# Performance work log

Hardware: AMD Instinct MI355X
Metric: run time of the kernel (lower is better)

## Reference

```python
import jax, jax.numpy as jnp
import numpy as np

KH, KW = 3, 3
STRIDE, PAD, DIL = 1, 1, 1
GROUPS, DG = 1, 1
B, C, H, W = 4, 64, 96, 96
O = 64
K = KH * KW


def setup_inputs() -> dict:
    key = jax.random.key(0)
    k1, k2, k3, k4 = jax.random.split(key, 4)
    x = jax.random.normal(k1, (B, C, H, W), dtype=jnp.float32)
    offset = jax.random.normal(k2, (B, DG * 2 * K, H, W), dtype=jnp.float32)
    mask = jax.random.uniform(k3, (B, DG * K, H, W), dtype=jnp.float32)
    stdv = 1.0 / np.sqrt(C * KH * KW)
    weight = jax.random.uniform(k4, (O, C // GROUPS, KH, KW), dtype=jnp.float32,
                                minval=-stdv, maxval=stdv)
    bias = jnp.zeros((O,), dtype=jnp.float32)
    return {"x": x, "offset": offset, "mask": mask, "weight": weight, "bias": bias}


def _dcn(x, offset, mask, weight, bias):
    Bc, Cc, Hc, Wc = x.shape
    Ho = (Hc + 2 * PAD - DIL * (KH - 1) - 1) // STRIDE + 1
    Wo = (Wc + 2 * PAD - DIL * (KW - 1) - 1) // STRIDE + 1
    Cg = Cc // DG
    dt = x.dtype

    # offset channels per deform group: [k, (y,x)] interleaved (mmcv layout)
    off = offset.reshape(Bc, DG, K, 2, Ho, Wo)
    off_y, off_x = off[:, :, :, 0], off[:, :, :, 1]          # [B,DG,K,Ho,Wo]
    m = mask.reshape(Bc, DG, K, Ho, Wo)

    ky = (jnp.arange(K) // KW).astype(dt) * DIL               # kernel tap dy
    kx = (jnp.arange(K) % KW).astype(dt) * DIL                # kernel tap dx
    base_y = (jnp.arange(Ho) * STRIDE - PAD).astype(dt)
    base_x = (jnp.arange(Wo) * STRIDE - PAD).astype(dt)
    py = base_y[None, None, None, :, None] + ky[None, None, :, None, None] + off_y
    px = base_x[None, None, None, None, :] + kx[None, None, :, None, None] + off_x

    y0 = jnp.floor(py)
    x0 = jnp.floor(px)
    ly = py - y0
    lx = px - x0
    y0i = y0.astype(jnp.int32)
    x0i = x0.astype(jnp.int32)

    x_flat = x.reshape(Bc, DG, Cg, Hc * Wc)

    def gather(yi, xi):
        # zero-padding semantics: out-of-range corners contribute 0
        valid = ((yi >= 0) & (yi < Hc) & (xi >= 0) & (xi < Wc)).astype(dt)
        idx = jnp.clip(yi, 0, Hc - 1) * Wc + jnp.clip(xi, 0, Wc - 1)
        idx_b = jnp.broadcast_to(idx.reshape(Bc, DG, 1, K * Ho * Wo),
                                 (Bc, DG, Cg, K * Ho * Wo))
        vals = jnp.take_along_axis(x_flat, idx_b, axis=3)
        return vals.reshape(Bc, DG, Cg, K, Ho, Wo), valid

    v00, m00 = gather(y0i, x0i)
    v01, m01 = gather(y0i, x0i + 1)
    v10, m10 = gather(y0i + 1, x0i)
    v11, m11 = gather(y0i + 1, x0i + 1)

    w00 = ((1 - ly) * (1 - lx) * m00)[:, :, None]             # [B,DG,1,K,Ho,Wo]
    w01 = ((1 - ly) * lx * m01)[:, :, None]
    w10 = (ly * (1 - lx) * m10)[:, :, None]
    w11 = (ly * lx * m11)[:, :, None]

    sampled = v00 * w00 + v01 * w01 + v10 * w10 + v11 * w11   # bilinear
    sampled = sampled * m[:, :, None]                         # mask modulation
    s = sampled.reshape(Bc, Cc, K, Ho, Wo)

    out = jnp.einsum('ock,bckhw->bohw', weight.reshape(O, Cc, K), s)
    return out + bias[None, :, None, None]


def reference(x, offset, mask, weight, bias):
    return _dcn(x, offset, mask, weight, bias)
```

## Files before the change

### kernel.cpp

```cpp
#include <hip/hip_runtime.h>

#define Bn 4
#define Cn 64
#define Hn 96
#define Wn 96
#define On 64
#define Kn 9
#define HWn (Hn*Wn)
#define NT 256
#define TW (Wn/16)
#define NTILES (Bn*Hn*TW)
#define NBLK (NTILES/4)

typedef __attribute__((ext_vector_type(8))) short bf16x8;
typedef __attribute__((ext_vector_type(4))) float f32x4;

__device__ __forceinline__ unsigned short f2bf(float f) {
    unsigned u = __float_as_uint(f);
    u += 0x7FFFu + ((u >> 16) & 1u);
    return (unsigned short)(u >> 16);
}
__device__ __forceinline__ float bf2f(unsigned short h) {
    return __uint_as_float((unsigned)h << 16);
}

__global__ void wtrans2_kernel(const float* __restrict__ w, unsigned short* __restrict__ wbfA) {
    int i = blockIdx.x * NT + threadIdx.x;
    if (i < 18 * 4 * 64 * 8) {
        int j  = i & 7;
        int l  = (i >> 3) & 63;
        int ot = (i >> 9) & 3;
        int t  = i >> 11;
        int o  = ot * 16 + (l & 15);
        int kp = t * 32 + (l >> 4) * 8 + j;
        wbfA[i] = f2bf(w[(o * Cn + (kp & 63)) * Kn + (kp >> 6)]);
    }
}

__global__ __launch_bounds__(NT) void xtrans_kernel(const float* __restrict__ x,
                                                    unsigned short* __restrict__ xT) {
    __shared__ unsigned short tile[Cn * Wn];
    const int tid = threadIdx.x;
    const int b = blockIdx.x / Hn;
    const int h = blockIdx.x - b * Hn;
    #pragma unroll
    for (int i = 0; i < (Cn * Wn) / NT; ++i) {
        int e = i * NT + tid;
        int c = e / Wn, w = e - c * Wn;
        tile[c * Wn + w] = f2bf(x[(((size_t)b * Cn + c) * Hn + h) * Wn + w]);
    }
    __syncthreads();
    #pragma unroll
    for (int i = 0; i < (Wn * 8) / NT; ++i) {
        int s = i * NT + tid;
        int w = s >> 3, g = s & 7;
        unsigned short hh[8];
        #pragma unroll
        for (int j = 0; j < 8; ++j) hh[j] = tile[(g * 8 + j) * Wn + w];
        uint4 pk;
        pk.x = hh[0] | ((unsigned)hh[1] << 16);
        pk.y = hh[2] | ((unsigned)hh[3] << 16);
        pk.z = hh[4] | ((unsigned)hh[5] << 16);
        pk.w = hh[6] | ((unsigned)hh[7] << 16);
        *(uint4*)&xT[(((size_t)b * Hn + h) * Wn + w) * Cn + g * 8] = pk;
    }
}

__global__ __launch_bounds__(NT) void dcn3_kernel(
    const unsigned short* __restrict__ xT, const float* __restrict__ offset,
    const float* __restrict__ mask, const float* __restrict__ bias,
    const unsigned short* __restrict__ wbfA, float* __restrict__ out)
{
    __shared__ float4 lwv[4 * Kn * 16];
    __shared__ int4   liv[4 * Kn * 16];

    const int tid = threadIdx.x;
    const int p = blockIdx.x;
    const int v = (p & 7) * (NBLK / 8) + (p >> 3);

    for (int e = tid; e < 4 * Kn * 16; e += NT) {
        int w   = e / (Kn * 16);
        int r   = e - w * (Kn * 16);
        int k   = r >> 4;
        int n   = r & 15;
        int T   = v * 4 + w;
        int b   = T / (Hn * TW);
        int rem = T - b * (Hn * TW);
        int ho  = rem / TW;
        int wt  = rem - ho * TW;
        int wo  = wt * 16 + n;

        float oy = offset[((b * (2*Kn) + 2*k    ) * Hn + ho) * Wn + wo];
        float ox = offset[((b * (2*Kn) + 2*k + 1) * Hn + ho) * Wn + wo];
        float mm = mask  [((b * Kn + k) * Hn + ho) * Wn + wo];
        float py = (float)(ho - 1 + (k / 3)) + oy;
        float px = (float)(wo - 1 + (k % 3)) + ox;
        float y0f = floorf(py), x0f = floorf(px);
        float ly = py - y0f, lx = px - x0f;
        int y0 = (int)y0f, x0i = (int)x0f;
        int y1 = y0 + 1,   x1i = x0i + 1;
        float vy0 = (y0  >= 0 && y0  < Hn) ? 1.f : 0.f;
        float vy1 = (y1  >= 0 && y1  < Hn) ? 1.f : 0.f;
        float vx0 = (x0i >= 0 && x0i < Wn) ? 1.f : 0.f;
        float vx1 = (x1i >= 0 && x1i < Wn) ? 1.f : 0.f;
        int cy0 = min(max(y0, 0),  Hn-1), cy1 = min(max(y1, 0),  Hn-1);
        int cx0 = min(max(x0i, 0), Wn-1), cx1 = min(max(x1i, 0), Wn-1);
        float4 wv;
        wv.x = (1.f - ly) * (1.f - lx) * mm * vy0 * vx0;
        wv.y = (1.f - ly) * lx         * mm * vy0 * vx1;
        wv.z = ly         * (1.f - lx) * mm * vy1 * vx0;
        wv.w = ly         * lx         * mm * vy1 * vx1;
        lwv[e] = wv;
        liv[e] = make_int4(cy0 * Wn + cx0, cy0 * Wn + cx1,
                           cy1 * Wn + cx0, cy1 * Wn + cx1);
    }
    __syncthreads();

    const int wave = tid >> 6;
    const int lane = tid & 63;
    const int n    = lane & 15;
    const int quad = lane >> 4;
    const int qo   = quad * 8;

    const int T  = v * 4 + wave;
    const int b  = T / (Hn * TW);
    int rem      = T - b * (Hn * TW);
    const int ho = rem / TW;
    const int wt = rem - ho * TW;
    const int wo0 = wt * 16;

    const unsigned short* xb = xT + (size_t)b * HWn * Cn;
    const bf16x8* Af = (const bf16x8*)wbfA;

    f32x4 acc[4] = {{0.f,0.f,0.f,0.f},{0.f,0.f,0.f,0.f},
                    {0.f,0.f,0.f,0.f},{0.f,0.f,0.f,0.f}};

    #pragma unroll
    for (int k = 0; k < Kn; ++k) {
        const int te = (wave * Kn + k) * 16 + n;
        float4 wv = lwv[te];
        int4   iv = liv[te];

        const unsigned short* r0 = xb + ((size_t)iv.x << 6) + qo;
        const unsigned short* r1 = xb + ((size_t)iv.y << 6) + qo;
        const unsigned short* r2 = xb + ((size_t)iv.z << 6) + qo;
        const unsigned short* r3 = xb + ((size_t)iv.w << 6) + qo;
        bf16x8 v00 = *(const bf16x8*)r0,  v01 = *(const bf16x8*)(r0 + 32);
        bf16x8 v10 = *(const bf16x8*)r1,  v11 = *(const bf16x8*)(r1 + 32);
        bf16x8 v20 = *(const bf16x8*)r2,  v21 = *(const bf16x8*)(r2 + 32);
        bf16x8 v30 = *(const bf16x8*)r3,  v31 = *(const bf16x8*)(r3 + 32);

        bf16x8 b0, b1;
        #pragma unroll
        for (int j = 0; j < 8; ++j) {
            float f0 = wv.x * bf2f((unsigned short)v00[j]) + wv.y * bf2f((unsigned short)v10[j])
                     + wv.z * bf2f((unsigned short)v20[j]) + wv.w * bf2f((unsigned short)v30[j]);
            float f1 = wv.x * bf2f((unsigned short)v01[j]) + wv.y * bf2f((unsigned short)v11[j])
                     + wv.z * bf2f((unsigned short)v21[j]) + wv.w * bf2f((unsigned short)v31[j]);
            b0[j] = (short)f2bf(f0);
            b1[j] = (short)f2bf(f1);
        }

        const int t0 = 2 * k, t1 = 2 * k + 1;
        #pragma unroll
        for (int ot = 0; ot < 4; ++ot) {
            bf16x8 a0 = Af[(t0 * 4 + ot) * 64 + lane];
            acc[ot] = __builtin_amdgcn_mfma_f32_16x16x32_bf16(a0, b0, acc[ot], 0, 0, 0);
        }
        #pragma unroll
        for (int ot = 0; ot < 4; ++ot) {
            bf16x8 a1 = Af[(t1 * 4 + ot) * 64 + lane];
            acc[ot] = __builtin_amdgcn_mfma_f32_16x16x32_bf16(a1, b1, acc[ot], 0, 0, 0);
        }
    }

    #pragma unroll
    for (int ot = 0; ot < 4; ++ot) {
        #pragma unroll
        for (int r = 0; r < 4; ++r) {
            int o = ot * 16 + quad * 4 + r;
            out[(((size_t)b * On + o) * Hn + ho) * Wn + wo0 + n] = acc[ot][r] + bias[o];
        }
    }
}

__global__ __launch_bounds__(NT) void dcn_fallback_kernel(
    const float* __restrict__ x, const float* __restrict__ offset,
    const float* __restrict__ mask, const float* __restrict__ weight,
    const float* __restrict__ bias, float* __restrict__ out)
{
    int idx = blockIdx.x * NT + threadIdx.x;
    if (idx >= Bn * On * HWn) return;
    int wo = idx % Wn;
    int ho = (idx / Wn) % Hn;
    int o  = (idx / HWn) % On;
    int b  = idx / (On * HWn);
    float s = bias[o];
    for (int k = 0; k < Kn; ++k) {
        float oy = offset[((b * (2*Kn) + 2*k    ) * Hn + ho) * Wn + wo];
        float ox = offset[((b * (2*Kn) + 2*k + 1) * Hn + ho) * Wn + wo];
        float mm = mask  [((b * Kn + k) * Hn + ho) * Wn + wo];
        float py = (float)(ho - 1 + (k / 3)) + oy;
        float px = (float)(wo - 1 + (k % 3)) + ox;
        float y0f = floorf(py), x0f = floorf(px);
        float ly = py - y0f, lx = px - x0f;
        int y0 = (int)y0f, x0i = (int)x0f, y1 = y0 + 1, x1i = x0i + 1;
        float vy0 = (y0  >= 0 && y0  < Hn) ? 1.f : 0.f;
        float vy1 = (y1  >= 0 && y1  < Hn) ? 1.f : 0.f;
        float vx0 = (x0i >= 0 && x0i < Wn) ? 1.f : 0.f;
        float vx1 = (x1i >= 0 && x1i < Wn) ? 1.f : 0.f;
        int cy0 = min(max(y0, 0),  Hn-1), cy1 = min(max(y1, 0),  Hn-1);
        int cx0 = min(max(x0i, 0), Wn-1), cx1 = min(max(x1i, 0), Wn-1);
        float w0 = (1.f-ly)*(1.f-lx)*mm*vy0*vx0, w1 = (1.f-ly)*lx*mm*vy0*vx1;
        float w2 = ly*(1.f-lx)*mm*vy1*vx0,       w3 = ly*lx*mm*vy1*vx1;
        int i0 = cy0*Wn+cx0, i1 = cy0*Wn+cx1, i2 = cy1*Wn+cx0, i3 = cy1*Wn+cx1;
        for (int c = 0; c < Cn; ++c) {
            const float* xp = x + ((size_t)b * Cn + c) * HWn;
            float vv = w0*xp[i0] + w1*xp[i1] + w2*xp[i2] + w3*xp[i3];
            s += vv * weight[(o * Cn + c) * Kn + k];
        }
    }
    out[idx] = s;
}

extern "C" void kernel_launch(void* const* d_in, const int* in_sizes, int n_in,
                              void* d_out, int out_size, void* d_ws, size_t ws_size,
                              hipStream_t stream) {
    const float* x      = (const float*)d_in[0];
    const float* offset = (const float*)d_in[1];
    const float* mask   = (const float*)d_in[2];
    const float* weight = (const float*)d_in[3];
    const float* bias   = (const float*)d_in[4];
    float* out = (float*)d_out;

    const size_t xt_bytes = (size_t)Bn * HWn * Cn * sizeof(unsigned short);
    const size_t w_bytes  = (size_t)18 * 4 * 64 * 8 * sizeof(unsigned short);

    if (ws_size >= xt_bytes + w_bytes) {
        unsigned short* xT   = (unsigned short*)d_ws;
        unsigned short* wbfA = (unsigned short*)((char*)d_ws + xt_bytes);
        wtrans2_kernel<<<(18*4*64*8 + NT - 1) / NT, NT, 0, stream>>>(weight, wbfA);
        xtrans_kernel<<<Bn * Hn, NT, 0, stream>>>(x, xT);
        dcn3_kernel<<<NBLK, NT, 0, stream>>>(xT, offset, mask, bias, wbfA, out);
    } else {
        dcn_fallback_kernel<<<(Bn * On * HWn + NT - 1) / NT, NT, 0, stream>>>(
            x, offset, mask, weight, bias, out);
    }
}
```

Measured before the change: 108.4 us.

## Split bilinear sampling across block into LDS tile, one output-channel group per wave

```diff
diff --git a/kernel.cpp b/kernel.cpp
--- a/kernel.cpp
+++ b/kernel.cpp
@@ -8,9 +8,11 @@
 #define Kn 9
 #define HWn (Hn*Wn)
 #define NT 256
-#define TW (Wn/16)
-#define NTILES (Bn*Hn*TW)
-#define NBLK (NTILES/4)
+#define TP 16
+#define TW (Wn/TP)
+#define NBLK (Bn*Hn*TW)
+#define SSTRIDE 584
+#define NWELEM (18*4*64*8)
 
 typedef __attribute__((ext_vector_type(8))) short bf16x8;
 typedef __attribute__((ext_vector_type(4))) float f32x4;
@@ -24,72 +26,72 @@
     return __uint_as_float((unsigned)h << 16);
 }
 
-__global__ void wtrans2_kernel(const float* __restrict__ w, unsigned short* __restrict__ wbfA) {
-    int i = blockIdx.x * NT + threadIdx.x;
-    if (i < 18 * 4 * 64 * 8) {
-        int j  = i & 7;
-        int l  = (i >> 3) & 63;
-        int ot = (i >> 9) & 3;
-        int t  = i >> 11;
-        int o  = ot * 16 + (l & 15);
-        int kp = t * 32 + (l >> 4) * 8 + j;
-        wbfA[i] = f2bf(w[(o * Cn + (kp & 63)) * Kn + (kp >> 6)]);
-    }
-}
-
-__global__ __launch_bounds__(NT) void xtrans_kernel(const float* __restrict__ x,
-                                                    unsigned short* __restrict__ xT) {
+__global__ __launch_bounds__(NT) void prep_kernel(
+    const float* __restrict__ x, const float* __restrict__ w,
+    unsigned short* __restrict__ xT, unsigned short* __restrict__ wbfA)
+{
     __shared__ unsigned short tile[Cn * Wn];
     const int tid = threadIdx.x;
-    const int b = blockIdx.x / Hn;
-    const int h = blockIdx.x - b * Hn;
-    #pragma unroll
-    for (int i = 0; i < (Cn * Wn) / NT; ++i) {
-        int e = i * NT + tid;
-        int c = e / Wn, w = e - c * Wn;
-        tile[c * Wn + w] = f2bf(x[(((size_t)b * Cn + c) * Hn + h) * Wn + w]);
-    }
-    __syncthreads();
-    #pragma unroll
-    for (int i = 0; i < (Wn * 8) / NT; ++i) {
-        int s = i * NT + tid;
-        int w = s >> 3, g = s & 7;
-        unsigned short hh[8];
+    if (blockIdx.x < Bn * Hn) {
+        const int b = blockIdx.x / Hn;
+        const int h = blockIdx.x - b * Hn;
         #pragma unroll
-        for (int j = 0; j < 8; ++j) hh[j] = tile[(g * 8 + j) * Wn + w];
-        uint4 pk;
-        pk.x = hh[0] | ((unsigned)hh[1] << 16);
-        pk.y = hh[2] | ((unsigned)hh[3] << 16);
-        pk.z = hh[4] | ((unsigned)hh[5] << 16);
-        pk.w = hh[6] | ((unsigned)hh[7] << 16);
-        *(uint4*)&xT[(((size_t)b * Hn + h) * Wn + w) * Cn + g * 8] = pk;
-    }
-}
-
-__global__ __launch_bounds__(NT) void dcn3_kernel(
+        for (int i = 0; i < (Cn * Wn) / NT; ++i) {
+            int e = i * NT + tid;
+            int c = e / Wn, ww = e - c * Wn;
+            tile[c * Wn + ww] = f2bf(x[(((size_t)b * Cn + c) * Hn + h) * Wn + ww]);
+        }
+        __syncthreads();
+        #pragma unroll
+        for (int i = 0; i < (Wn * 8) / NT; ++i) {
+            int s = i * NT + tid;
+            int ww = s >> 3, g = s & 7;
+            unsigned short hh[8];
+            #pragma unroll
+            for (int j = 0; j < 8; ++j) hh[j] = tile[(g * 8 + j) * Wn + ww];
+            uint4 pk;
+            pk.x = hh[0] | ((unsigned)hh[1] << 16);
+            pk.y = hh[2] | ((unsigned)hh[3] << 16);
+            pk.z = hh[4] | ((unsigned)hh[5] << 16);
+            pk.w = hh[6] | ((unsigned)hh[7] << 16);
+            *(uint4*)&xT[(((size_t)b * Hn + h) * Wn + ww) * Cn + g * 8] = pk;
+        }
+    } else {
+        int i = (blockIdx.x - Bn * Hn) * NT + tid;
+        if (i < NWELEM) {
+            int j  = i & 7;
+            int l  = (i >> 3) & 63;
+            int wv = (i >> 9) & 3;
+            int t  = i >> 11;
+            int o  = wv * 16 + (l & 15);
+            int kp = t * 32 + (l >> 4) * 8 + j;
+            wbfA[i] = f2bf(w[(o * Cn + (kp & 63)) * Kn + (kp >> 6)]);
+        }
+    }
+}
+
+__global__ __launch_bounds__(NT, 6) void dcn4_kernel(
     const unsigned short* __restrict__ xT, const float* __restrict__ offset,
     const float* __restrict__ mask, const float* __restrict__ bias,
     const unsigned short* __restrict__ wbfA, float* __restrict__ out)
 {
-    __shared__ float4 lwv[4 * Kn * 16];
-    __shared__ int4   liv[4 * Kn * 16];
+    __shared__ float4 lwv[Kn * TP];
+    __shared__ int4   liv[Kn * TP];
+    __shared__ __align__(16) unsigned short Slds[TP * SSTRIDE];
 
     const int tid = threadIdx.x;
     const int p = blockIdx.x;
     const int v = (p & 7) * (NBLK / 8) + (p >> 3);
-
-    for (int e = tid; e < 4 * Kn * 16; e += NT) {
-        int w   = e / (Kn * 16);
-        int r   = e - w * (Kn * 16);
-        int k   = r >> 4;
-        int n   = r & 15;
-        int T   = v * 4 + w;
-        int b   = T / (Hn * TW);
-        int rem = T - b * (Hn * TW);
-        int ho  = rem / TW;
-        int wt  = rem - ho * TW;
-        int wo  = wt * 16 + n;
-
+    const int b  = v / (Hn * TW);
+    int rem      = v - b * (Hn * TW);
+    const int ho = rem / TW;
+    const int wt = rem - ho * TW;
+    const int wo0 = wt * TP;
+
+    if (tid < Kn * TP) {
+        int k = tid >> 4;
+        int n = tid & 15;
+        int wo = wo0 + n;
         float oy = offset[((b * (2*Kn) + 2*k    ) * Hn + ho) * Wn + wo];
         float ox = offset[((b * (2*Kn) + 2*k + 1) * Hn + ho) * Wn + wo];
         float mm = mask  [((b * Kn + k) * Hn + ho) * Wn + wo];
@@ -110,77 +112,69 @@
         wv.y = (1.f - ly) * lx         * mm * vy0 * vx1;
         wv.z = ly         * (1.f - lx) * mm * vy1 * vx0;
         wv.w = ly         * lx         * mm * vy1 * vx1;
-        lwv[e] = wv;
-        liv[e] = make_int4(cy0 * Wn + cx0, cy0 * Wn + cx1,
-                           cy1 * Wn + cx0, cy1 * Wn + cx1);
+        lwv[tid] = wv;
+        liv[tid] = make_int4(cy0 * Wn + cx0, cy0 * Wn + cx1,
+                             cy1 * Wn + cx0, cy1 * Wn + cx1);
     }
     __syncthreads();
+
+    {
+        const int px = tid >> 4;
+        const int g  = tid & 7;
+        const int hf = (tid >> 3) & 1;
+        const unsigned short* xb = xT + (size_t)b * HWn * Cn + g * 8;
+        #pragma unroll
+        for (int k = 0; k < Kn; ++k) {
+            const int e = k * TP + px;
+            float4 wv = lwv[e];
+            int4   iv = liv[e];
+            int   ia = hf ? iv.z : iv.x;
+            int   ib = hf ? iv.w : iv.y;
+            float wa = hf ? wv.z : wv.x;
+            float wb = hf ? wv.w : wv.y;
+            bf16x8 va = *(const bf16x8*)(xb + ((size_t)ia << 6));
+            bf16x8 vb = *(const bf16x8*)(xb + ((size_t)ib << 6));
+            unsigned short hh[8];
+            #pragma unroll
+            for (int j = 0; j < 8; ++j) {
+                float f = wa * bf2f((unsigned short)va[j]) + wb * bf2f((unsigned short)vb[j]);
+                f += __shfl_xor(f, 8);
+                hh[j] = f2bf(f);
+            }
+            if (hf == 0) {
+                uint4 pk;
+                pk.x = hh[0] | ((unsigned)hh[1] << 16);
+                pk.y = hh[2] | ((unsigned)hh[3] << 16);
+                pk.z = hh[4] | ((unsigned)hh[5] << 16);
+                pk.w = hh[6] | ((unsigned)hh[7] << 16);
+                *(uint4*)&Slds[px * SSTRIDE + k * 64 + g * 8] = pk;
+            }
+        }
+    }
 
     const int wave = tid >> 6;
     const int lane = tid & 63;
     const int n    = lane & 15;
     const int quad = lane >> 4;
-    const int qo   = quad * 8;
-
-    const int T  = v * 4 + wave;
-    const int b  = T / (Hn * TW);
-    int rem      = T - b * (Hn * TW);
-    const int ho = rem / TW;
-    const int wt = rem - ho * TW;
-    const int wo0 = wt * 16;
-
-    const unsigned short* xb = xT + (size_t)b * HWn * Cn;
     const bf16x8* Af = (const bf16x8*)wbfA;
-
-    f32x4 acc[4] = {{0.f,0.f,0.f,0.f},{0.f,0.f,0.f,0.f},
-                    {0.f,0.f,0.f,0.f},{0.f,0.f,0.f,0.f}};
-
+    bf16x8 aCur = Af[(0 * 4 + wave) * 64 + lane];
+    bf16x8 aNxt = Af[(1 * 4 + wave) * 64 + lane];
+    __syncthreads();
+
+    f32x4 acc = {0.f, 0.f, 0.f, 0.f};
     #pragma unroll
-    for (int k = 0; k < Kn; ++k) {
-        const int te = (wave * Kn + k) * 16 + n;
-        float4 wv = lwv[te];
-        int4   iv = liv[te];
-
-        const unsigned short* r0 = xb + ((size_t)iv.x << 6) + qo;
-        const unsigned short* r1 = xb + ((size_t)iv.y << 6) + qo;
-        const unsigned short* r2 = xb + ((size_t)iv.z << 6) + qo;
-        const unsigned short* r3 = xb + ((size_t)iv.w << 6) + qo;
-        bf16x8 v00 = *(const bf16x8*)r0,  v01 = *(const bf16x8*)(r0 + 32);
-        bf16x8 v10 = *(const bf16x8*)r1,  v11 = *(const bf16x8*)(r1 + 32);
-        bf16x8 v20 = *(const bf16x8*)r2,  v21 = *(const bf16x8*)(r2 + 32);
-        bf16x8 v30 = *(const bf16x8*)r3,  v31 = *(const bf16x8*)(r3 + 32);
-
-        bf16x8 b0, b1;
-        #pragma unroll
-        for (int j = 0; j < 8; ++j) {
-            float f0 = wv.x * bf2f((unsigned short)v00[j]) + wv.y * bf2f((unsigned short)v10[j])
-                     + wv.z * bf2f((unsigned short)v20[j]) + wv.w * bf2f((unsigned short)v30[j]);
-            float f1 = wv.x * bf2f((unsigned short)v01[j]) + wv.y * bf2f((unsigned short)v11[j])
-                     + wv.z * bf2f((unsigned short)v21[j]) + wv.w * bf2f((unsigned short)v31[j]);
-            b0[j] = (short)f2bf(f0);
-            b1[j] = (short)f2bf(f1);
-        }
-
-        const int t0 = 2 * k, t1 = 2 * k + 1;
-        #pragma unroll
-        for (int ot = 0; ot < 4; ++ot) {
-            bf16x8 a0 = Af[(t0 * 4 + ot) * 64 + lane];
-            acc[ot] = __builtin_amdgcn_mfma_f32_16x16x32_bf16(a0, b0, acc[ot], 0, 0, 0);
-        }
-        #pragma unroll
-        for (int ot = 0; ot < 4; ++ot) {
-            bf16x8 a1 = Af[(t1 * 4 + ot) * 64 + lane];
-            acc[ot] = __builtin_amdgcn_mfma_f32_16x16x32_bf16(a1, b1, acc[ot], 0, 0, 0);
-        }
+    for (int t = 0; t < 18; ++t) {
+        bf16x8 aUse = aCur;
+        aCur = aNxt;
+        if (t < 16) aNxt = Af[((t + 2) * 4 + wave) * 64 + lane];
+        bf16x8 bfr = *(const bf16x8*)&Slds[n * SSTRIDE + t * 32 + quad * 8];
+        acc = __builtin_amdgcn_mfma_f32_16x16x32_bf16(aUse, bfr, acc, 0, 0, 0);
     }
 
     #pragma unroll
-    for (int ot = 0; ot < 4; ++ot) {
-        #pragma unroll
-        for (int r = 0; r < 4; ++r) {
-            int o = ot * 16 + quad * 4 + r;
-            out[(((size_t)b * On + o) * Hn + ho) * Wn + wo0 + n] = acc[ot][r] + bias[o];
-        }
+    for (int r = 0; r < 4; ++r) {
+        int o = wave * 16 + quad * 4 + r;
+        out[(((size_t)b * On + o) * Hn + ho) * Wn + wo0 + n] = acc[r] + bias[o];
     }
 }
 
@@ -234,14 +228,13 @@
     float* out = (float*)d_out;
 
     const size_t xt_bytes = (size_t)Bn * HWn * Cn * sizeof(unsigned short);
-    const size_t w_bytes  = (size_t)18 * 4 * 64 * 8 * sizeof(unsigned short);
+    const size_t w_bytes  = (size_t)NWELEM * sizeof(unsigned short);
 
     if (ws_size >= xt_bytes + w_bytes) {
         unsigned short* xT   = (unsigned short*)d_ws;
         unsigned short* wbfA = (unsigned short*)((char*)d_ws + xt_bytes);
-        wtrans2_kernel<<<(18*4*64*8 + NT - 1) / NT, NT, 0, stream>>>(weight, wbfA);
-        xtrans_kernel<<<Bn * Hn, NT, 0, stream>>>(x, xT);
-        dcn3_kernel<<<NBLK, NT, 0, stream>>>(xT, offset, mask, bias, wbfA, out);
+        prep_kernel<<<Bn * Hn + (NWELEM + NT - 1) / NT, NT, 0, stream>>>(x, weight, xT, wbfA);
+        dcn4_kernel<<<NBLK, NT, 0, stream>>>(xT, offset, mask, bias, wbfA, out);
     } else {
         dcn_fallback_kernel<<<(Bn * On * HWn + NT - 1) / NT, NT, 0, stream>>>(
             x, offset, mask, weight, bias, out);
```

Measured after the change: 91.73 us. 15.4% less time.
